# Performance work log

Measured on AMD Instinct MI355X. Metric: run time of the kernel, lower is better.

Reference implementation:

```python
import jax, jax.numpy as jnp
import numpy as np

NUM_PERIODS = 24


def setup_inputs() -> dict:
    key = jax.random.key(0)
    ks = jax.random.split(key, 12)
    B, N, F, H, E = 32, 1024, 128, 64, 16
    scale = 1.0 / np.sqrt(F)
    inp = {
        "input_features": jax.random.normal(ks[0], (B, N, F), jnp.float32),
        "cycle_indices": jax.random.randint(ks[1], (B,), 0, NUM_PERIODS, jnp.int64),
        "weight": jax.random.normal(ks[2], (F, F), jnp.float32) * scale,
        "bias": jnp.zeros((F,), jnp.float32),
        "src_emb": jax.random.normal(ks[3], (NUM_PERIODS, N, H), jnp.float32) * 0.1,
        "tgt_emb": jax.random.normal(ks[4], (NUM_PERIODS, N, H), jnp.float32) * 0.1,
        "env_W": jax.random.normal(ks[5], (E, H), jnp.float32) * (1.0 / np.sqrt(E)),
        "env_b": jnp.zeros((H,), jnp.float32),
        "res_W": jax.random.normal(ks[6], (F, F), jnp.float32) * scale,
        "res_b": jnp.zeros((F,), jnp.float32),
        "static_adj": (jax.random.uniform(ks[7], (N, N)) < 0.05).astype(jnp.float32),
        "env_features": jax.random.normal(ks[8], (N, E), jnp.float32),
    }
    return inp


def reference(input_features, cycle_indices, weight, bias, src_emb, tgt_emb,
              env_W, env_b, res_W, res_b, static_adj, env_features):
    # env encoder: Linear + ReLU (dropout is identity at inference)
    env_emb = jax.nn.relu(env_features @ env_W + env_b)            # [N, H]

    # per-period adaptive adjacency, masked by static sparsity pattern
    src = src_emb + env_emb                                        # [P, N, H]
    tgt = tgt_emb + env_emb                                        # [P, N, H]
    scores = jnp.einsum('pnh,pmh->pnm', src, tgt)                  # [P, N, N]
    adj = jax.nn.relu(scores) * static_adj                         # [P, N, N]

    period = (cycle_indices % NUM_PERIODS).astype(jnp.int32)       # [B]
    adj_b = adj[period]                                            # [B, N, N]

    support = jnp.einsum('bnd,dm->bnm', input_features, weight)    # [B, N, F]
    convolved = jnp.einsum('bnm,bmf->bnf', adj_b, support) + bias  # [B, N, F]

    residual = jax.nn.relu(input_features @ res_W + res_b)         # [B, N, F]
    return jax.nn.relu(convolved + residual)
```

## Files before the change

### kernel.cpp

```cpp
#include <hip/hip_runtime.h>
#include <hip/hip_bf16.h>

#define NPER 24
#define B_ 32
#define N_ 1024
#define F_ 128
#define H_ 64
#define E_ 16

typedef __attribute__((ext_vector_type(8))) short short8;
typedef __attribute__((ext_vector_type(4))) float f32x4;

#define GLD16(g, l) __builtin_amdgcn_global_load_lds( \
    (const __attribute__((address_space(1))) void*)(g), \
    (__attribute__((address_space(3))) void*)(l), 16, 0, 0)

static __device__ __forceinline__ unsigned short f2bf(float x) {
    union { float f; unsigned u; } v; v.f = x;
    unsigned r = v.u + 0x7fffu + ((v.u >> 16) & 1u);
    return (unsigned short)(r >> 16);
}
static __device__ __forceinline__ float bf2f(unsigned short h) {
    union { unsigned u; float f; } v; v.u = ((unsigned)h) << 16; return v.f;
}
static __device__ __forceinline__ unsigned short f2bf_hw(float x) {
    __hip_bfloat16 h = __float2bfloat16(x);
    return *(unsigned short*)&h;
}

__global__ __launch_bounds__(256) void prep_all(
    const float* __restrict__ src_emb, const float* __restrict__ tgt_emb,
    const float* __restrict__ env_features, const float* __restrict__ env_W,
    const float* __restrict__ env_b,
    const float* __restrict__ adj, const float* __restrict__ W,
    const float* __restrict__ rW,
    unsigned short* __restrict__ src_bf, unsigned short* __restrict__ tgt_bf,
    unsigned short* __restrict__ adj_bf, unsigned short* __restrict__ Wt,
    unsigned short* __restrict__ rWt)
{
    const int bid = blockIdx.x;
    if (bid < 256) {
        const int idx = bid * 256 + threadIdx.x;
        const int n = idx >> 6, h = idx & 63;
        float e = env_b[h];
#pragma unroll
        for (int k = 0; k < E_; ++k)
            e = fmaf(env_features[n * E_ + k], env_W[k * H_ + h], e);
        e = fmaxf(e, 0.f);
#pragma unroll 4
        for (int p = 0; p < NPER; ++p) {
            const size_t off = (size_t)p * (N_ * H_) + idx;
            src_bf[off] = f2bf(src_emb[off] + e);
            tgt_bf[off] = f2bf(tgt_emb[off] + e);
        }
    } else if (bid < 1280) {
        const size_t i = ((size_t)(bid - 256) * 256 + threadIdx.x) * 4;
        float4 v = *(const float4*)(adj + i);
        ushort4 o;
        o.x = f2bf(v.x); o.y = f2bf(v.y); o.z = f2bf(v.z); o.w = f2bf(v.w);
        *(ushort4*)(adj_bf + i) = o;
    } else {
        const int idx = (bid - 1280) * 256 + threadIdx.x;
        const int which = idx >> 14, j = idx & 16383;
        const int f = j >> 7, d = j & 127;
        if (which == 0) Wt[f * 128 + d]  = f2bf(W[d * 128 + f]);
        else            rWt[f * 128 + d] = f2bf(rW[d * 128 + f]);
    }
}

__global__ __launch_bounds__(256) void gemm2_mfma(
    const float* __restrict__ x,
    const unsigned short* __restrict__ Wt,
    const unsigned short* __restrict__ rWt,
    const float* __restrict__ rb,
    unsigned short* __restrict__ supT,
    unsigned short* __restrict__ resid)
{
    const int t = threadIdx.x, w = t >> 6, l = t & 63;
    const int ln = l & 15, kb = l >> 4;
    const int mblk = w >> 1, fhalf = w & 1;
    const int row0 = blockIdx.x * 32;
    const int b   = row0 >> 10;
    const int mg0 = row0 & 1023;

    const float* xrow = x + (size_t)(row0 + mblk * 16 + ln) * 128;
    short8 xa[4];
#pragma unroll
    for (int k = 0; k < 4; ++k) {
        float4 v0 = *(const float4*)(xrow + k * 32 + kb * 8);
        float4 v1 = *(const float4*)(xrow + k * 32 + kb * 8 + 4);
        short8 s;
        s[0] = (short)f2bf(v0.x); s[1] = (short)f2bf(v0.y);
        s[2] = (short)f2bf(v0.z); s[3] = (short)f2bf(v0.w);
        s[4] = (short)f2bf(v1.x); s[5] = (short)f2bf(v1.y);
        s[6] = (short)f2bf(v1.z); s[7] = (short)f2bf(v1.w);
        xa[k] = s;
    }

    f32x4 accS[4], accR[4];
#pragma unroll
    for (int i = 0; i < 4; ++i) { accS[i] = (f32x4){0,0,0,0}; accR[i] = (f32x4){0,0,0,0}; }

#pragma unroll
    for (int k = 0; k < 4; ++k) {
#pragma unroll
        for (int fb = 0; fb < 4; ++fb) {
            int fr = (fhalf * 4 + fb) * 16 + ln;
            short8 wa = *(const short8*)(Wt  + (size_t)fr * 128 + k * 32 + kb * 8);
            short8 wb = *(const short8*)(rWt + (size_t)fr * 128 + k * 32 + kb * 8);
            accS[fb] = __builtin_amdgcn_mfma_f32_16x16x32_bf16(wa, xa[k], accS[fb], 0, 0, 0);
            accR[fb] = __builtin_amdgcn_mfma_f32_16x16x32_bf16(xa[k], wb, accR[fb], 0, 0, 0);
        }
    }

#pragma unroll
    for (int fb = 0; fb < 4; ++fb) {
        int m = mg0 + mblk * 16 + ln;
#pragma unroll
        for (int i = 0; i < 4; ++i) {
            int f = (fhalf * 4 + fb) * 16 + kb * 4 + i;
            supT[((size_t)b * 128 + f) * 1024 + m] = f2bf(accS[fb][i]);
        }
    }
#pragma unroll
    for (int fb = 0; fb < 4; ++fb) {
        int f = (fhalf * 4 + fb) * 16 + ln;
        float rbf = rb[f];
#pragma unroll
        for (int i = 0; i < 4; ++i) {
            size_t row = (size_t)row0 + mblk * 16 + kb * 4 + i;
            resid[row * 128 + f] = f2bf(fmaxf(accR[fb][i] + rbf, 0.f));
        }
    }
}

__global__ __launch_bounds__(256, 2) void conv_mfma(
    const unsigned short* __restrict__ src_bf,
    const unsigned short* __restrict__ tgt_bf,
    const unsigned short* __restrict__ adj_bf,
    const unsigned short* __restrict__ supT,
    const unsigned short* __restrict__ resid,
    const float* __restrict__ bias,
    const int* __restrict__ cyc,
    float* __restrict__ out)
{
    __shared__ unsigned short s_tgt[2][64 * 64] __attribute__((aligned(16)));
    __shared__ unsigned short s_sup[2][128 * 64] __attribute__((aligned(16)));
    __shared__ unsigned short s_a[64][72] __attribute__((aligned(16)));

    const int i = blockIdx.x;
    const int work = (i & 7) * 64 + (i >> 3);
    const int b  = work >> 4;
    const int n0 = (work & 15) * 64;

    const int t = threadIdx.x, w = t >> 6, l = t & 63;
    const int ln = l & 15, kb = l >> 4;
    const int p = ((cyc[b] % NPER) + NPER) % NPER;

    const int sn = w >> 1, sm = w & 1;
    const int cf = w;

    short8 sfrag[2][2];
#pragma unroll
    for (int nt = 0; nt < 2; ++nt)
#pragma unroll
        for (int k2 = 0; k2 < 2; ++k2)
            sfrag[nt][k2] = *(const short8*)(
                src_bf + ((size_t)p * N_ + n0 + sn * 32 + nt * 16 + ln) * H_ + k2 * 32 + kb * 8);

    const unsigned short* tgtg = tgt_bf + (size_t)p * N_ * H_;
    const unsigned short* supg = supT + (size_t)b * F_ * N_;

    f32x4 acc[4][2];
#pragma unroll
    for (int q = 0; q < 4; ++q)
#pragma unroll
        for (int fb = 0; fb < 2; ++fb) acc[q][fb] = (f32x4){0, 0, 0, 0};

    auto stage = [&](int buf, int m0) {
#pragma unroll
        for (int j = 0; j < 2; ++j) {
            const int te = j * 256 + t;
            GLD16(tgtg + (size_t)(m0 + (te >> 3)) * H_ + (te & 7) * 8,
                  &s_tgt[buf][te * 8]);
        }
#pragma unroll
        for (int j = 0; j < 4; ++j) {
            const int te = j * 256 + t;
            GLD16(supg + (size_t)(te >> 3) * N_ + m0 + (te & 7) * 8,
                  &s_sup[buf][te * 8]);
        }
    };

    auto loadAdj = [&](int m0, ushort4 (&av)[2][2]) {
#pragma unroll
        for (int nt = 0; nt < 2; ++nt)
#pragma unroll
            for (int mt = 0; mt < 2; ++mt)
                av[nt][mt] = *(const ushort4*)(
                    adj_bf + (size_t)(n0 + sn * 32 + nt * 16 + ln) * N_
                           + m0 + sm * 32 + mt * 16 + kb * 4);
    };

    auto score = [&](int buf, const ushort4 (&av)[2][2]) {
        short8 tf[2][2];
#pragma unroll
        for (int mt = 0; mt < 2; ++mt)
#pragma unroll
            for (int k2 = 0; k2 < 2; ++k2)
                tf[mt][k2] = *(const short8*)(
                    &s_tgt[buf][(sm * 32 + mt * 16 + ln) * H_ + k2 * 32 + kb * 8]);
#pragma unroll
        for (int nt = 0; nt < 2; ++nt)
#pragma unroll
            for (int mt = 0; mt < 2; ++mt) {
                f32x4 c = (f32x4){0, 0, 0, 0};
                c = __builtin_amdgcn_mfma_f32_16x16x32_bf16(tf[mt][0], sfrag[nt][0], c, 0, 0, 0);
                c = __builtin_amdgcn_mfma_f32_16x16x32_bf16(tf[mt][1], sfrag[nt][1], c, 0, 0, 0);
                const int nl = sn * 32 + nt * 16 + ln;
                const int ml = sm * 32 + mt * 16 + kb * 4;
                const ushort4 a = av[nt][mt];
                uint2 q;
                q.x = (unsigned)f2bf_hw(fmaxf(c[0], 0.f) * bf2f(a.x))
                    | ((unsigned)f2bf_hw(fmaxf(c[1], 0.f) * bf2f(a.y)) << 16);
                q.y = (unsigned)f2bf_hw(fmaxf(c[2], 0.f) * bf2f(a.z))
                    | ((unsigned)f2bf_hw(fmaxf(c[3], 0.f) * bf2f(a.w)) << 16);
                *(uint2*)(&s_a[nl][ml]) = q;
            }
    };

    auto conv = [&](int buf) {
#pragma unroll
        for (int ks = 0; ks < 2; ++ks) {
            short8 bfrag[2];
#pragma unroll
            for (int fb = 0; fb < 2; ++fb)
                bfrag[fb] = *(const short8*)(
                    &s_sup[buf][(cf * 32 + fb * 16 + ln) * 64 + ks * 32 + kb * 8]);
#pragma unroll
            for (int nt2 = 0; nt2 < 4; ++nt2) {
                short8 af = *(const short8*)(&s_a[nt2 * 16 + ln][ks * 32 + kb * 8]);
#pragma unroll
                for (int fb = 0; fb < 2; ++fb)
                    acc[nt2][fb] = __builtin_amdgcn_mfma_f32_16x16x32_bf16(
                        af, bfrag[fb], acc[nt2][fb], 0, 0, 0);
            }
        }
    };

    auto bar_lgkm = []() {
        asm volatile("s_waitcnt lgkmcnt(0)" ::: "memory");
        __builtin_amdgcn_s_barrier();
    };
    auto bar_vm0 = []() {
        asm volatile("s_waitcnt vmcnt(0) lgkmcnt(0)" ::: "memory");
        __builtin_amdgcn_s_barrier();
    };

    ushort4 avA[2][2], avB[2][2];

    stage(0, 0);
    loadAdj(0, avA);
    bar_vm0();

    for (int tt = 0; tt < 16; tt += 2) {
        stage(1, (tt + 1) * 64);
        loadAdj((tt + 1) * 64, avB);
        score(0, avA);
        bar_lgkm();
        conv(0);
        bar_vm0();

        if (tt + 2 < 16) {
            stage(0, (tt + 2) * 64);
            loadAdj((tt + 2) * 64, avA);
        }
        score(1, avB);
        bar_lgkm();
        conv(1);
        bar_vm0();
    }

#pragma unroll
    for (int nt2 = 0; nt2 < 4; ++nt2)
#pragma unroll
    for (int fb = 0; fb < 2; ++fb) {
        const int f = cf * 32 + fb * 16 + ln;
        const float bi = bias[f];
#pragma unroll
        for (int ii = 0; ii < 4; ++ii) {
            const int n = n0 + nt2 * 16 + kb * 4 + ii;
            const size_t o = ((size_t)b * N_ + n) * F_ + f;
            out[o] = fmaxf(acc[nt2][fb][ii] + bi + bf2f(resid[o]), 0.f);
        }
    }
}

extern "C" void kernel_launch(void* const* d_in, const int* in_sizes, int n_in,
                              void* d_out, int out_size, void* d_ws, size_t ws_size,
                              hipStream_t stream) {
    const float* input_features = (const float*)d_in[0];
    const int*   cycle_indices  = (const int*)  d_in[1];
    const float* weight         = (const float*)d_in[2];
    const float* bias           = (const float*)d_in[3];
    const float* src_emb        = (const float*)d_in[4];
    const float* tgt_emb        = (const float*)d_in[5];
    const float* env_W          = (const float*)d_in[6];
    const float* env_b          = (const float*)d_in[7];
    const float* res_W          = (const float*)d_in[8];
    const float* res_b          = (const float*)d_in[9];
    const float* static_adj     = (const float*)d_in[10];
    const float* env_features   = (const float*)d_in[11];
    float* out = (float*)d_out;

    char* wsb = (char*)d_ws;
    unsigned short* src_bf = (unsigned short*)wsb;
    unsigned short* tgt_bf = src_bf + (size_t)NPER * N_ * H_;
    unsigned short* Wt     = tgt_bf + (size_t)NPER * N_ * H_;
    unsigned short* rWt    = Wt + 16384;
    unsigned short* supT   = rWt + 16384;
    unsigned short* resid  = supT + (size_t)B_ * F_ * N_;
    unsigned short* adj_bf = resid + (size_t)B_ * N_ * F_;

    prep_all<<<1408, 256, 0, stream>>>(
        src_emb, tgt_emb, env_features, env_W, env_b,
        static_adj, weight, res_W,
        src_bf, tgt_bf, adj_bf, Wt, rWt);

    gemm2_mfma<<<(B_ * N_) / 32, 256, 0, stream>>>(
        input_features, Wt, rWt, res_b, supT, resid);

    conv_mfma<<<512, 256, 0, stream>>>(
        src_bf, tgt_bf, adj_bf, supT, resid, bias, cycle_indices, out);
}
```

Measured before the change: 65.53 us.

## Shrink conv tile to 32 rows with per-wave score tiles and swizzled LDS

Halves the conv kernel's node tile from 64 to 32 rows and the K step from 64 to 32, doubling the grid to 1024 blocks and raising launch bounds to 4 blocks per CU. Each wave now computes its own 16-row score tile in a private LDS slice, which removes the intermediate barrier between score and conv. XOR swizzles are added to the tgt and support LDS layouts to avoid bank conflicts. The aim is more occupancy and fewer barriers, but each block recomputes scores redundantly (each wave pair duplicates the score computation across F halves) and reuses support and tgt data less.

```diff
diff --git a/kernel.cpp b/kernel.cpp
--- a/kernel.cpp
+++ b/kernel.cpp
@@ -134,7 +134,7 @@
     }
 }
 
-__global__ __launch_bounds__(256, 2) void conv_mfma(
+__global__ __launch_bounds__(256, 4) void conv_mfma(
     const unsigned short* __restrict__ src_bf,
     const unsigned short* __restrict__ tgt_bf,
     const unsigned short* __restrict__ adj_bf,
@@ -144,154 +144,125 @@
     const int* __restrict__ cyc,
     float* __restrict__ out)
 {
-    __shared__ unsigned short s_tgt[2][64 * 64] __attribute__((aligned(16)));
-    __shared__ unsigned short s_sup[2][128 * 64] __attribute__((aligned(16)));
-    __shared__ unsigned short s_a[64][72] __attribute__((aligned(16)));
+    __shared__ unsigned short s_tgt[2][32 * 64] __attribute__((aligned(16)));
+    __shared__ unsigned short s_sup[2][128 * 32] __attribute__((aligned(16)));
+    __shared__ unsigned short s_a[4][16 * 40] __attribute__((aligned(16)));
 
     const int i = blockIdx.x;
-    const int work = (i & 7) * 64 + (i >> 3);
-    const int b  = work >> 4;
-    const int n0 = (work & 15) * 64;
+    const int work = (i & 7) * 128 + (i >> 3);
+    const int b  = work >> 5;
+    const int n0 = (work & 31) * 32;
 
     const int t = threadIdx.x, w = t >> 6, l = t & 63;
     const int ln = l & 15, kb = l >> 4;
+    const int ns = w & 1;
+    const int fh = w >> 1;
     const int p = ((cyc[b] % NPER) + NPER) % NPER;
 
-    const int sn = w >> 1, sm = w & 1;
-    const int cf = w;
-
-    short8 sfrag[2][2];
-#pragma unroll
-    for (int nt = 0; nt < 2; ++nt)
-#pragma unroll
-        for (int k2 = 0; k2 < 2; ++k2)
-            sfrag[nt][k2] = *(const short8*)(
-                src_bf + ((size_t)p * N_ + n0 + sn * 32 + nt * 16 + ln) * H_ + k2 * 32 + kb * 8);
+    const unsigned short* srow =
+        src_bf + ((size_t)p * N_ + n0 + ns * 16 + ln) * H_;
+    short8 sfrag[2];
+    sfrag[0] = *(const short8*)(srow + kb * 8);
+    sfrag[1] = *(const short8*)(srow + 32 + kb * 8);
 
     const unsigned short* tgtg = tgt_bf + (size_t)p * N_ * H_;
     const unsigned short* supg = supT + (size_t)b * F_ * N_;
-
-    f32x4 acc[4][2];
-#pragma unroll
-    for (int q = 0; q < 4; ++q)
-#pragma unroll
-        for (int fb = 0; fb < 2; ++fb) acc[q][fb] = (f32x4){0, 0, 0, 0};
+    const unsigned short* adjp = adj_bf + (size_t)(n0 + ns * 16 + ln) * N_;
+    unsigned short* saw = &s_a[w][0];
+
+    f32x4 acc[4];
+#pragma unroll
+    for (int q = 0; q < 4; ++q) acc[q] = (f32x4){0, 0, 0, 0};
 
     auto stage = [&](int buf, int m0) {
+        {
+            const int r = t >> 3, c = t & 7;
+            GLD16(tgtg + (size_t)(m0 + r) * H_ + (c ^ (r & 7)) * 8,
+                  &s_tgt[buf][t * 8]);
+        }
 #pragma unroll
         for (int j = 0; j < 2; ++j) {
             const int te = j * 256 + t;
-            GLD16(tgtg + (size_t)(m0 + (te >> 3)) * H_ + (te & 7) * 8,
-                  &s_tgt[buf][te * 8]);
-        }
-#pragma unroll
-        for (int j = 0; j < 4; ++j) {
-            const int te = j * 256 + t;
-            GLD16(supg + (size_t)(te >> 3) * N_ + m0 + (te & 7) * 8,
+            const int r = te >> 2, c = te & 3;
+            GLD16(supg + (size_t)r * N_ + m0 + (c ^ ((r >> 1) & 3)) * 8,
                   &s_sup[buf][te * 8]);
         }
     };
 
-    auto loadAdj = [&](int m0, ushort4 (&av)[2][2]) {
-#pragma unroll
-        for (int nt = 0; nt < 2; ++nt)
-#pragma unroll
-            for (int mt = 0; mt < 2; ++mt)
-                av[nt][mt] = *(const ushort4*)(
-                    adj_bf + (size_t)(n0 + sn * 32 + nt * 16 + ln) * N_
-                           + m0 + sm * 32 + mt * 16 + kb * 4);
-    };
-
-    auto score = [&](int buf, const ushort4 (&av)[2][2]) {
-        short8 tf[2][2];
+    auto loadAdj = [&](int m0, ushort4 (&av)[2]) {
 #pragma unroll
         for (int mt = 0; mt < 2; ++mt)
-#pragma unroll
-            for (int k2 = 0; k2 < 2; ++k2)
-                tf[mt][k2] = *(const short8*)(
-                    &s_tgt[buf][(sm * 32 + mt * 16 + ln) * H_ + k2 * 32 + kb * 8]);
-#pragma unroll
-        for (int nt = 0; nt < 2; ++nt)
-#pragma unroll
-            for (int mt = 0; mt < 2; ++mt) {
-                f32x4 c = (f32x4){0, 0, 0, 0};
-                c = __builtin_amdgcn_mfma_f32_16x16x32_bf16(tf[mt][0], sfrag[nt][0], c, 0, 0, 0);
-                c = __builtin_amdgcn_mfma_f32_16x16x32_bf16(tf[mt][1], sfrag[nt][1], c, 0, 0, 0);
-                const int nl = sn * 32 + nt * 16 + ln;
-                const int ml = sm * 32 + mt * 16 + kb * 4;
-                const ushort4 a = av[nt][mt];
-                uint2 q;
-                q.x = (unsigned)f2bf_hw(fmaxf(c[0], 0.f) * bf2f(a.x))
-                    | ((unsigned)f2bf_hw(fmaxf(c[1], 0.f) * bf2f(a.y)) << 16);
-                q.y = (unsigned)f2bf_hw(fmaxf(c[2], 0.f) * bf2f(a.z))
-                    | ((unsigned)f2bf_hw(fmaxf(c[3], 0.f) * bf2f(a.w)) << 16);
-                *(uint2*)(&s_a[nl][ml]) = q;
-            }
+            av[mt] = *(const ushort4*)(adjp + m0 + mt * 16 + kb * 4);
+    };
+
+    auto score = [&](int buf, const ushort4 (&av)[2]) {
+#pragma unroll
+        for (int mt = 0; mt < 2; ++mt) {
+            const int trow = mt * 16 + ln;
+            short8 tf0 = *(const short8*)(
+                &s_tgt[buf][trow * 64 + ((kb) ^ (trow & 7)) * 8]);
+            short8 tf1 = *(const short8*)(
+                &s_tgt[buf][trow * 64 + ((4 + kb) ^ (trow & 7)) * 8]);
+            f32x4 c = (f32x4){0, 0, 0, 0};
+            c = __builtin_amdgcn_mfma_f32_16x16x32_bf16(tf0, sfrag[0], c, 0, 0, 0);
+            c = __builtin_amdgcn_mfma_f32_16x16x32_bf16(tf1, sfrag[1], c, 0, 0, 0);
+            const ushort4 a = av[mt];
+            uint2 q;
+            q.x = (unsigned)f2bf_hw(fmaxf(c[0], 0.f) * bf2f(a.x))
+                | ((unsigned)f2bf_hw(fmaxf(c[1], 0.f) * bf2f(a.y)) << 16);
+            q.y = (unsigned)f2bf_hw(fmaxf(c[2], 0.f) * bf2f(a.z))
+                | ((unsigned)f2bf_hw(fmaxf(c[3], 0.f) * bf2f(a.w)) << 16);
+            *(uint2*)(saw + ln * 40 + mt * 16 + kb * 4) = q;
+        }
     };
 
     auto conv = [&](int buf) {
-#pragma unroll
-        for (int ks = 0; ks < 2; ++ks) {
-            short8 bfrag[2];
-#pragma unroll
-            for (int fb = 0; fb < 2; ++fb)
-                bfrag[fb] = *(const short8*)(
-                    &s_sup[buf][(cf * 32 + fb * 16 + ln) * 64 + ks * 32 + kb * 8]);
-#pragma unroll
-            for (int nt2 = 0; nt2 < 4; ++nt2) {
-                short8 af = *(const short8*)(&s_a[nt2 * 16 + ln][ks * 32 + kb * 8]);
-#pragma unroll
-                for (int fb = 0; fb < 2; ++fb)
-                    acc[nt2][fb] = __builtin_amdgcn_mfma_f32_16x16x32_bf16(
-                        af, bfrag[fb], acc[nt2][fb], 0, 0, 0);
-            }
-        }
-    };
-
-    auto bar_lgkm = []() {
-        asm volatile("s_waitcnt lgkmcnt(0)" ::: "memory");
-        __builtin_amdgcn_s_barrier();
-    };
+        short8 af = *(const short8*)(saw + ln * 40 + kb * 8);
+#pragma unroll
+        for (int fb = 0; fb < 4; ++fb) {
+            const int frow = fh * 64 + fb * 16 + ln;
+            short8 bfrag = *(const short8*)(
+                &s_sup[buf][frow * 32 + ((kb) ^ ((frow >> 1) & 3)) * 8]);
+            acc[fb] = __builtin_amdgcn_mfma_f32_16x16x32_bf16(af, bfrag, acc[fb], 0, 0, 0);
+        }
+    };
+
     auto bar_vm0 = []() {
         asm volatile("s_waitcnt vmcnt(0) lgkmcnt(0)" ::: "memory");
         __builtin_amdgcn_s_barrier();
     };
 
-    ushort4 avA[2][2], avB[2][2];
+    ushort4 avA[2], avB[2];
 
     stage(0, 0);
     loadAdj(0, avA);
     bar_vm0();
 
-    for (int tt = 0; tt < 16; tt += 2) {
-        stage(1, (tt + 1) * 64);
-        loadAdj((tt + 1) * 64, avB);
+    for (int tt = 0; tt < 32; tt += 2) {
+        stage(1, (tt + 1) * 32);
+        loadAdj((tt + 1) * 32, avB);
         score(0, avA);
-        bar_lgkm();
         conv(0);
         bar_vm0();
 
-        if (tt + 2 < 16) {
-            stage(0, (tt + 2) * 64);
-            loadAdj((tt + 2) * 64, avA);
+        if (tt + 2 < 32) {
+            stage(0, (tt + 2) * 32);
+            loadAdj((tt + 2) * 32, avA);
         }
         score(1, avB);
-        bar_lgkm();
         conv(1);
         bar_vm0();
     }
 
 #pragma unroll
-    for (int nt2 = 0; nt2 < 4; ++nt2)
-#pragma unroll
-    for (int fb = 0; fb < 2; ++fb) {
-        const int f = cf * 32 + fb * 16 + ln;
+    for (int fb = 0; fb < 4; ++fb) {
+        const int f = fh * 64 + fb * 16 + ln;
         const float bi = bias[f];
 #pragma unroll
         for (int ii = 0; ii < 4; ++ii) {
-            const int n = n0 + nt2 * 16 + kb * 4 + ii;
+            const int n = n0 + ns * 16 + kb * 4 + ii;
             const size_t o = ((size_t)b * N_ + n) * F_ + f;
-            out[o] = fmaxf(acc[nt2][fb][ii] + bi + bf2f(resid[o]), 0.f);
+            out[o] = fmaxf(acc[fb][ii] + bi + bf2f(resid[o]), 0.f);
         }
     }
 }
@@ -330,6 +301,6 @@
     gemm2_mfma<<<(B_ * N_) / 32, 256, 0, stream>>>(
         input_features, Wt, rWt, res_b, supT, resid);
 
-    conv_mfma<<<512, 256, 0, stream>>>(
+    conv_mfma<<<1024, 256, 0, stream>>>(
         src_bf, tgt_bf, adj_bf, supT, resid, bias, cycle_indices, out);
 }
```

Measured after the change: 81.35 us. +24.1%, slower.
